# Kernel tuning notes

Hardware: AMD Instinct MI355X
Metric: run time of the kernel (lower is better)

The kernel has to match this reference:

```python
import jax, jax.numpy as jnp
import numpy as np

N_SPK, N_UTT, D_EMB = 1024, 20, 512
COS_EPS = 1e-8   # torch F.cosine_similarity default eps
SIM_EPS = 1e-6   # added to cosine and inside the log, per original code


def setup_inputs() -> dict:
    key = jax.random.key(0)
    embeddings = jax.random.normal(key, (N_SPK, N_UTT, D_EMB), dtype=jnp.float32)
    w = jnp.asarray(10.0, dtype=jnp.float32)
    b = jnp.asarray(-5.0, dtype=jnp.float32)
    return {"embeddings": embeddings, "w": w, "b": b}


def reference(embeddings, w, b):
    N, M, D = embeddings.shape
    sums = embeddings.sum(axis=1)                       # [N, D]
    centroids = sums / M                                # [N, D] full centroids
    cent_excl = (sums[:, None, :] - embeddings) / (M - 1)  # [N, M, D] leave-one-out

    def _norm(x):
        return x / jnp.maximum(jnp.linalg.norm(x, axis=-1, keepdims=True), COS_EPS)

    e_n = _norm(embeddings)          # [N, M, D]
    c_n = _norm(centroids)           # [N, D]
    ce_n = _norm(cent_excl)          # [N, M, D]

    # cosine vs every speaker centroid
    cs = jnp.einsum('nmd,kd->nmk', e_n, c_n)            # [N, M, N]
    # replace same-speaker column with leave-one-out cosine
    diag = jnp.sum(e_n * ce_n, axis=-1)                 # [N, M]
    same = jnp.eye(N, dtype=bool)[:, None, :]           # [N, 1, N]
    cossim = jnp.where(same, diag[:, :, None], cs) + SIM_EPS

    sim = w * cossim + b                                # [N, M, N]
    pos = w * (diag + SIM_EPS) + b                      # sim[j, i, j]
    lse = jnp.log(jnp.sum(jnp.exp(sim), axis=-1) + SIM_EPS)  # [N, M]
    loss = jnp.sum(lse - pos)
    return loss
```

## Files before the change

### kernel.cpp

```cpp
#include <hip/hip_runtime.h>
#include <hip/hip_bf16.h>

typedef unsigned short u16;
typedef unsigned int u32;
typedef unsigned char u8;
typedef int i32x8 __attribute__((ext_vector_type(8)));
typedef float f32x4 __attribute__((ext_vector_type(4)));

#define NSPK 1024
#define NUTT 20
#define DEMB 512
#define NROW (NSPK * NUTT)

__device__ __forceinline__ uint2 pk_fp8x8(float a, float b, float c, float d,
                                          float e, float f, float g, float h) {
    int lo = __builtin_amdgcn_cvt_pk_fp8_f32(a, b, 0, 0);
    lo = __builtin_amdgcn_cvt_pk_fp8_f32(c, d, lo, 1);
    int hi = __builtin_amdgcn_cvt_pk_fp8_f32(e, f, 0, 0);
    hi = __builtin_amdgcn_cvt_pk_fp8_f32(g, h, hi, 1);
    return make_uint2((u32)lo, (u32)hi);
}

__global__ __launch_bounds__(256) void prep_f(const float* __restrict__ E,
                                              u8* __restrict__ A,
                                              u8* __restrict__ Bc,
                                              float* __restrict__ diag,
                                              float* __restrict__ csd,
                                              float* __restrict__ out) {
    __shared__ float sbuf[4][DEMB];
    const int t = threadIdx.x, lane = t & 63, wv = t >> 6;
    const int n = blockIdx.x;
    const float* Eb = E + (size_t)n * (NUTT * DEMB) + (size_t)(wv * 5) * DEMB + lane * 8;

    float4 e0[5], e1[5];
    float4 p0 = {0, 0, 0, 0}, p1 = {0, 0, 0, 0};
#pragma unroll
    for (int i = 0; i < 5; ++i) {
        e0[i] = *(const float4*)(Eb + (size_t)i * DEMB);
        e1[i] = *(const float4*)(Eb + (size_t)i * DEMB + 4);
        p0.x += e0[i].x; p0.y += e0[i].y; p0.z += e0[i].z; p0.w += e0[i].w;
        p1.x += e1[i].x; p1.y += e1[i].y; p1.z += e1[i].z; p1.w += e1[i].w;
    }
    *(float4*)(&sbuf[wv][lane * 8])     = p0;
    *(float4*)(&sbuf[wv][lane * 8 + 4]) = p1;
    __syncthreads();

    float4 s0 = {0, 0, 0, 0}, s1 = {0, 0, 0, 0};
#pragma unroll
    for (int k = 0; k < 4; ++k) {
        float4 a = *(const float4*)(&sbuf[k][lane * 8]);
        float4 b = *(const float4*)(&sbuf[k][lane * 8 + 4]);
        s0.x += a.x; s0.y += a.y; s0.z += a.z; s0.w += a.w;
        s1.x += b.x; s1.y += b.y; s1.z += b.z; s1.w += b.w;
    }

    float ls = s0.x*s0.x + s0.y*s0.y + s0.z*s0.z + s0.w*s0.w
             + s1.x*s1.x + s1.y*s1.y + s1.z*s1.z + s1.w*s1.w;
#pragma unroll
    for (int o = 32; o; o >>= 1) ls += __shfl_xor(ls, o);
    const float ss = ls;
    const float rc = 1.0f / fmaxf(sqrtf(ss) * 0.05f, 1e-8f);
    const float g  = rc * 0.05f;

    ((uint2*)(Bc + (size_t)n * DEMB))[lane] =
        pk_fp8x8(s0.x * g, s0.y * g, s0.z * g, s0.w * g,
                 s1.x * g, s1.y * g, s1.z * g, s1.w * g);

#pragma unroll
    for (int i = 0; i < 5; ++i) {
        float ee = e0[i].x*e0[i].x + e0[i].y*e0[i].y + e0[i].z*e0[i].z + e0[i].w*e0[i].w
                 + e1[i].x*e1[i].x + e1[i].y*e1[i].y + e1[i].z*e1[i].z + e1[i].w*e1[i].w;
        float es = e0[i].x*s0.x + e0[i].y*s0.y + e0[i].z*s0.z + e0[i].w*s0.w
                 + e1[i].x*s1.x + e1[i].y*s1.y + e1[i].z*s1.z + e1[i].w*s1.w;
#pragma unroll
        for (int o = 32; o; o >>= 1) { ee += __shfl_xor(ee, o); es += __shfl_xor(es, o); }

        const float rne = 1.0f / fmaxf(sqrtf(ee), 1e-8f);
        const float pxx = ss - 2.f * es + ee;
        const float dg  = (es - ee) * rne / fmaxf(sqrtf(pxx), 1.9e-7f);

        const int r = n * NUTT + wv * 5 + i;
        ((uint2*)(A + (size_t)r * DEMB))[lane] =
            pk_fp8x8(e0[i].x * rne, e0[i].y * rne, e0[i].z * rne, e0[i].w * rne,
                     e1[i].x * rne, e1[i].y * rne, e1[i].z * rne, e1[i].w * rne);
        if (lane == 0) {
            diag[r] = dg;
            csd[r]  = es * g * rne;
        }
    }

    if (n == 0 && t == 0) out[0] = 0.f;
}

__device__ __forceinline__ void async_copy16(const void* g, void* l) {
    __builtin_amdgcn_global_load_lds(
        (const __attribute__((address_space(1))) void*)g,
        (__attribute__((address_space(3))) void*)l, 16, 0, 0);
}

__global__ __launch_bounds__(256, 1) void gemm_fin(const u8* __restrict__ A,
                                                   const u8* __restrict__ Bc,
                                                   const float* __restrict__ wp,
                                                   const float* __restrict__ bp,
                                                   const float* __restrict__ diag,
                                                   const float* __restrict__ csd,
                                                   float* __restrict__ out) {
    __shared__ u8 As[80 * DEMB];
    __shared__ u8 Bs[2][128 * 128];
    __shared__ float red[4][80];
    __shared__ float s_red[4];
    const int t = threadIdx.x, lane = t & 63, wv = t >> 6;
    const int ml = lane & 15, q = lane >> 4;
    const int blk = blockIdx.x;
    const u8* Ag = A + (size_t)blk * 80 * DEMB;

    const float w = *wp, bb = *bp;
    asm volatile("s_waitcnt vmcnt(0) lgkmcnt(0)" ::: "memory");

    int boff[4];
#pragma unroll
    for (int j = 0; j < 4; ++j) {
        const int c = t + 256 * j;
        const int r = c >> 3, kg = (c & 7) ^ (r & 7);
        boff[j] = r * DEMB + kg * 16;
    }

    auto stageB = [&](int tileN, int kt, u8* buf) {
#pragma unroll
        for (int j = 0; j < 4; ++j)
            async_copy16(Bc + (size_t)tileN * (128 * DEMB) + kt * 128 + boff[j],
                         buf + t * 16 + j * 4096);
    };

#pragma unroll
    for (int jj = 0; jj < 10; ++jj) {
        const int c = t + 256 * jj;
        const int r = c >> 5, sl = c & 31;
        async_copy16(Ag + (size_t)r * DEMB + ((sl ^ (r & 31)) << 4),
                     As + t * 16 + jj * 4096);
    }
    stageB(0, 0, Bs[0]);
    stageB(0, 1, Bs[1]);
    asm volatile("s_waitcnt vmcnt(4)" ::: "memory");
    __builtin_amdgcn_sched_barrier(0);
    __builtin_amdgcn_s_barrier();
    __builtin_amdgcn_sched_barrier(0);

    i32x8 a[5][4];
#pragma unroll
    for (int m = 0; m < 5; ++m) {
        const int r = m * 16 + ml;
#pragma unroll
        for (int kt = 0; kt < 4; ++kt) {
            const int sl0 = (kt * 8 + 2 * q)     ^ (r & 31);
            const int sl1 = (kt * 8 + 2 * q + 1) ^ (r & 31);
            uint4 x = *(const uint4*)(As + r * DEMB + (sl0 << 4));
            uint4 y = *(const uint4*)(As + r * DEMB + (sl1 << 4));
            a[m][kt] = (i32x8){(int)x.x, (int)x.y, (int)x.z, (int)x.w,
                               (int)y.x, (int)y.y, (int)y.z, (int)y.w};
        }
    }
    asm volatile("s_waitcnt lgkmcnt(0)" ::: "memory");
    __builtin_amdgcn_sched_barrier(0);

    f32x4 acc[5][2], rowpart[5];
#pragma unroll
    for (int m = 0; m < 5; ++m) {
        acc[m][0] = (f32x4){0.f, 0.f, 0.f, 0.f};
        acc[m][1] = (f32x4){0.f, 0.f, 0.f, 0.f};
        rowpart[m] = (f32x4){0.f, 0.f, 0.f, 0.f};
    }

    int bo0[2], bo1[2];
#pragma unroll
    for (int nf = 0; nf < 2; ++nf) {
        const int c = wv * 32 + nf * 16 + ml;
        bo0[nf] = c * 128 + (((2 * q)     ^ (c & 7)) << 4);
        bo1[nf] = c * 128 + (((2 * q + 1) ^ (c & 7)) << 4);
    }

    for (int tileN = 0; tileN < 8; ++tileN) {
#pragma unroll
        for (int kt = 0; kt < 4; ++kt) {
            const u8* bufc = Bs[kt & 1];
            i32x8 bf[2];
#pragma unroll
            for (int nf = 0; nf < 2; ++nf) {
                uint4 x = *(const uint4*)(bufc + bo0[nf]);
                uint4 y = *(const uint4*)(bufc + bo1[nf]);
                bf[nf] = (i32x8){(int)x.x, (int)x.y, (int)x.z, (int)x.w,
                                 (int)y.x, (int)y.y, (int)y.z, (int)y.w};
            }
            asm volatile("s_waitcnt lgkmcnt(0)" ::: "memory");
            __builtin_amdgcn_sched_barrier(0);
#pragma unroll
            for (int m = 0; m < 5; ++m)
#pragma unroll
                for (int nf = 0; nf < 2; ++nf)
                    acc[m][nf] = __builtin_amdgcn_mfma_scale_f32_16x16x128_f8f6f4(
                        a[m][kt], bf[nf], acc[m][nf], 0, 0,
                        0, 0x7F7F7F7F, 0, 0x7F7F7F7F);

            __builtin_amdgcn_sched_barrier(0);
            __builtin_amdgcn_s_barrier();
            __builtin_amdgcn_sched_barrier(0);

            if (kt < 2 || tileN < 7)
                stageB(tileN + (kt >= 2), (kt + 2) & 3, (u8*)Bs[kt & 1]);

            if (kt == 3) {
#pragma unroll
                for (int m = 0; m < 5; ++m) {
#pragma unroll
                    for (int r = 0; r < 4; ++r)
                        rowpart[m][r] += __expf(fmaf(w, acc[m][0][r] + 1e-6f, bb))
                                       + __expf(fmaf(w, acc[m][1][r] + 1e-6f, bb));
                    acc[m][0] = (f32x4){0.f, 0.f, 0.f, 0.f};
                    acc[m][1] = (f32x4){0.f, 0.f, 0.f, 0.f};
                }
            }

            if (kt == 2) {
                if (tileN == 7) { asm volatile("s_waitcnt vmcnt(0)" ::: "memory"); }
                else           { asm volatile("s_waitcnt vmcnt(4)" ::: "memory"); }
                __builtin_amdgcn_sched_barrier(0);
                __builtin_amdgcn_s_barrier();
                __builtin_amdgcn_sched_barrier(0);
            } else if (kt == 3) {
                if (tileN < 7) {
                    asm volatile("s_waitcnt vmcnt(4)" ::: "memory");
                    __builtin_amdgcn_sched_barrier(0);
                    __builtin_amdgcn_s_barrier();
                    __builtin_amdgcn_sched_barrier(0);
                }
            } else {
                asm volatile("s_waitcnt vmcnt(4)" ::: "memory");
                __builtin_amdgcn_sched_barrier(0);
                __builtin_amdgcn_s_barrier();
                __builtin_amdgcn_sched_barrier(0);
            }
        }
    }

#pragma unroll
    for (int m = 0; m < 5; ++m)
#pragma unroll
        for (int o = 1; o < 16; o <<= 1) {
            rowpart[m][0] += __shfl_xor(rowpart[m][0], o);
            rowpart[m][1] += __shfl_xor(rowpart[m][1], o);
            rowpart[m][2] += __shfl_xor(rowpart[m][2], o);
            rowpart[m][3] += __shfl_xor(rowpart[m][3], o);
        }
    if (ml == 0) {
#pragma unroll
        for (int m = 0; m < 5; ++m)
#pragma unroll
            for (int r = 0; r < 4; ++r)
                red[wv][m * 16 + q * 4 + r] = rowpart[m][r];
    }
    __syncthreads();

    float term = 0.f;
    if (t < 80) {
        const float rsum = red[0][t] + red[1][t] + red[2][t] + red[3][t];
        const int row = blk * 80 + t;
        const float pos = fmaf(w, diag[row] + 1e-6f, bb);
        const float S = rsum - __expf(fmaf(w, csd[row] + 1e-6f, bb)) + __expf(pos);
        term = __logf(S + 1e-6f) - pos;
    }
#pragma unroll
    for (int o = 32; o; o >>= 1) term += __shfl_xor(term, o);
    if (lane == 0) s_red[wv] = term;
    __syncthreads();
    if (t == 0) atomicAdd(out, s_red[0] + s_red[1] + s_red[2] + s_red[3]);
}

extern "C" void kernel_launch(void* const* d_in, const int* in_sizes, int n_in,
                              void* d_out, int out_size, void* d_ws, size_t ws_size,
                              hipStream_t stream) {
    const float* E = (const float*)d_in[0];
    const float* wp = (const float*)d_in[1];
    const float* bp = (const float*)d_in[2];
    float* out = (float*)d_out;

    char* ws = (char*)d_ws;
    u8* A      = (u8*)(ws);
    u8* Bc     = (u8*)(ws + 10485760);
    float* dg  = (float*)(ws + 11010048);
    float* cs  = (float*)(ws + 11091968);

    prep_f<<<NSPK, 256, 0, stream>>>(E, A, Bc, dg, cs, out);
    gemm_fin<<<256, 256, 0, stream>>>(A, Bc, wp, bp, dg, cs, out);
}
```

Baseline: 107.9 us.

## Give each wave private B staging buffers and drop block barriers from GEMM loop

Each wave now stages only the 32 B columns it consumes into its own double-buffered LDS region, so the per-k-step block-wide s_barriers are replaced by per-wave vmcnt waits. B fragments for the next step are loaded into registers before the current MFMAs issue, which prefetches LDS reads. The loop is fully unrolled over 32 steps. This removes cross-wave synchronization stalls, but it relies on each wave's own waitcnt being enough to see its async-copied LDS data, and the full unroll increases code size and register pressure.

New measurement: 105.2 us. -2.5%, faster.

```diff
diff --git a/kernel.cpp b/kernel.cpp
--- a/kernel.cpp
+++ b/kernel.cpp
@@ -106,7 +106,7 @@
                                                    const float* __restrict__ csd,
                                                    float* __restrict__ out) {
     __shared__ u8 As[80 * DEMB];
-    __shared__ u8 Bs[2][128 * 128];
+    __shared__ u8 Bls[4][2][4096];
     __shared__ float red[4][80];
     __shared__ float s_red[4];
     const int t = threadIdx.x, lane = t & 63, wv = t >> 6;
@@ -115,22 +115,6 @@
     const u8* Ag = A + (size_t)blk * 80 * DEMB;
 
     const float w = *wp, bb = *bp;
-    asm volatile("s_waitcnt vmcnt(0) lgkmcnt(0)" ::: "memory");
-
-    int boff[4];
-#pragma unroll
-    for (int j = 0; j < 4; ++j) {
-        const int c = t + 256 * j;
-        const int r = c >> 3, kg = (c & 7) ^ (r & 7);
-        boff[j] = r * DEMB + kg * 16;
-    }
-
-    auto stageB = [&](int tileN, int kt, u8* buf) {
-#pragma unroll
-        for (int j = 0; j < 4; ++j)
-            async_copy16(Bc + (size_t)tileN * (128 * DEMB) + kt * 128 + boff[j],
-                         buf + t * 16 + j * 4096);
-    };
 
 #pragma unroll
     for (int jj = 0; jj < 10; ++jj) {
@@ -139,9 +123,28 @@
         async_copy16(Ag + (size_t)r * DEMB + ((sl ^ (r & 31)) << 4),
                      As + t * 16 + jj * 4096);
     }
-    stageB(0, 0, Bs[0]);
-    stageB(0, 1, Bs[1]);
-    asm volatile("s_waitcnt vmcnt(4)" ::: "memory");
+
+    const int C0 = wv * 256;
+    int rj[4], kg16[4];
+#pragma unroll
+    for (int j = 0; j < 4; ++j) {
+        const int c = lane + 64 * j;
+        rj[j] = c >> 3;
+        kg16[j] = ((c & 7) ^ (rj[j] & 7)) << 4;
+    }
+
+#define STAGEB(U, KT, PAR)                                                    \
+    {                                                                         \
+        _Pragma("unroll")                                                     \
+        for (int j = 0; j < 4; ++j)                                           \
+            async_copy16(Bc + (size_t)(C0 + (U) * 32 + rj[j]) * DEMB +        \
+                             (KT) * 128 + kg16[j],                            \
+                         &Bls[wv][PAR][j * 1024 + lane * 16]);                \
+    }
+
+    STAGEB(0, 0, 0);
+    STAGEB(0, 1, 1);
+    asm volatile("s_waitcnt vmcnt(8)" ::: "memory");
     __builtin_amdgcn_sched_barrier(0);
     __builtin_amdgcn_s_barrier();
     __builtin_amdgcn_sched_barrier(0);
@@ -160,8 +163,6 @@
                                (int)y.x, (int)y.y, (int)y.z, (int)y.w};
         }
     }
-    asm volatile("s_waitcnt lgkmcnt(0)" ::: "memory");
-    __builtin_amdgcn_sched_barrier(0);
 
     f32x4 acc[5][2], rowpart[5];
 #pragma unroll
@@ -174,40 +175,50 @@
     int bo0[2], bo1[2];
 #pragma unroll
     for (int nf = 0; nf < 2; ++nf) {
-        const int c = wv * 32 + nf * 16 + ml;
-        bo0[nf] = c * 128 + (((2 * q)     ^ (c & 7)) << 4);
-        bo1[nf] = c * 128 + (((2 * q + 1) ^ (c & 7)) << 4);
-    }
-
-    for (int tileN = 0; tileN < 8; ++tileN) {
+        const int cc = nf * 16 + ml;
+        bo0[nf] = cc * 128 + (((2 * q)     ^ (cc & 7)) << 4);
+        bo1[nf] = cc * 128 + (((2 * q + 1) ^ (cc & 7)) << 4);
+    }
+
+    i32x8 bf[2][2];
+#define LOADBF(PAR)                                                           \
+    {                                                                         \
+        _Pragma("unroll")                                                     \
+        for (int nf = 0; nf < 2; ++nf) {                                      \
+            uint4 x = *(const uint4*)(&Bls[wv][PAR][bo0[nf]]);                \
+            uint4 y = *(const uint4*)(&Bls[wv][PAR][bo1[nf]]);                \
+            bf[PAR][nf] = (i32x8){(int)x.x, (int)x.y, (int)x.z, (int)x.w,     \
+                                  (int)y.x, (int)y.y, (int)y.z, (int)y.w};    \
+        }                                                                     \
+    }
+
+    asm volatile("s_waitcnt vmcnt(4)" ::: "memory");
+    __builtin_amdgcn_sched_barrier(0);
+    LOADBF(0);
+
+#pragma unroll
+    for (int u = 0; u < 8; ++u) {
 #pragma unroll
         for (int kt = 0; kt < 4; ++kt) {
-            const u8* bufc = Bs[kt & 1];
-            i32x8 bf[2];
-#pragma unroll
-            for (int nf = 0; nf < 2; ++nf) {
-                uint4 x = *(const uint4*)(bufc + bo0[nf]);
-                uint4 y = *(const uint4*)(bufc + bo1[nf]);
-                bf[nf] = (i32x8){(int)x.x, (int)x.y, (int)x.z, (int)x.w,
-                                 (int)y.x, (int)y.y, (int)y.z, (int)y.w};
-            }
+            const int s = u * 4 + kt, par = s & 1;
             asm volatile("s_waitcnt lgkmcnt(0)" ::: "memory");
             __builtin_amdgcn_sched_barrier(0);
+            if (s + 2 < 32) {
+                const int s2 = s + 2;
+                STAGEB(s2 >> 2, s2 & 3, par);
+            }
+            __builtin_amdgcn_sched_barrier(0);
+            if (s == 30)      { asm volatile("s_waitcnt vmcnt(0)" ::: "memory"); }
+            else if (s < 30)  { asm volatile("s_waitcnt vmcnt(4)" ::: "memory"); }
+            __builtin_amdgcn_sched_barrier(0);
+            if (s < 31) LOADBF(par ^ 1);
 #pragma unroll
             for (int m = 0; m < 5; ++m)
 #pragma unroll
                 for (int nf = 0; nf < 2; ++nf)
                     acc[m][nf] = __builtin_amdgcn_mfma_scale_f32_16x16x128_f8f6f4(
-                        a[m][kt], bf[nf], acc[m][nf], 0, 0,
+                        a[m][kt], bf[par][nf], acc[m][nf], 0, 0,
                         0, 0x7F7F7F7F, 0, 0x7F7F7F7F);
-
-            __builtin_amdgcn_sched_barrier(0);
-            __builtin_amdgcn_s_barrier();
-            __builtin_amdgcn_sched_barrier(0);
-
-            if (kt < 2 || tileN < 7)
-                stageB(tileN + (kt >= 2), (kt + 2) & 3, (u8*)Bs[kt & 1]);
-
             if (kt == 3) {
 #pragma unroll
                 for (int m = 0; m < 5; ++m) {
@@ -219,28 +230,10 @@
                     acc[m][1] = (f32x4){0.f, 0.f, 0.f, 0.f};
                 }
             }
-
-            if (kt == 2) {
-                if (tileN == 7) { asm volatile("s_waitcnt vmcnt(0)" ::: "memory"); }
-                else           { asm volatile("s_waitcnt vmcnt(4)" ::: "memory"); }
-                __builtin_amdgcn_sched_barrier(0);
-                __builtin_amdgcn_s_barrier();
-                __builtin_amdgcn_sched_barrier(0);
-            } else if (kt == 3) {
-                if (tileN < 7) {
-                    asm volatile("s_waitcnt vmcnt(4)" ::: "memory");
-                    __builtin_amdgcn_sched_barrier(0);
-                    __builtin_amdgcn_s_barrier();
-                    __builtin_amdgcn_sched_barrier(0);
-                }
-            } else {
-                asm volatile("s_waitcnt vmcnt(4)" ::: "memory");
-                __builtin_amdgcn_sched_barrier(0);
-                __builtin_amdgcn_s_barrier();
-                __builtin_amdgcn_sched_barrier(0);
-            }
-        }
-    }
+        }
+    }
+#undef STAGEB
+#undef LOADBF
 
 #pragma unroll
     for (int m = 0; m < 5; ++m)
```
